# Optimization experiments

Measured on AMD Instinct MI355X. Metric: run time of the kernel, lower is better.

The kernel has to match this reference:

```python
import jax, jax.numpy as jnp
import numpy as np

B, N_GENES, N_SETS, G = 256, 10000, 1000, 128   # batch, input_dim, output_dim, geneset_size
H1, H2 = 64, 32                                  # hidden_dims
EPS = 1e-5                                       # BatchNorm1d eps


def _batchnorm(h, gamma, beta):
    # BatchNorm1d in training mode: biased batch stats over the batch axis
    mean = jnp.mean(h, axis=0, keepdims=True)
    var = jnp.mean(jnp.square(h - mean), axis=0, keepdims=True)
    return (h - mean) * jax.lax.rsqrt(var + EPS) * gamma + beta


def setup_inputs() -> dict:
    key = jax.random.key(0)
    ks = jax.random.split(key, 7)
    # Adjacency with exactly G distinct ones per column -> gather index list [N_SETS, G]
    rng = np.random.default_rng(0)
    gene_idx = np.argsort(rng.random((N_SETS, N_GENES)), axis=1)[:, :G]
    gene_idx = jnp.asarray(np.sort(gene_idx, axis=1), dtype=jnp.int32)

    x = jax.random.normal(ks[0], (B, N_GENES), jnp.float32)
    s1, s2, s3 = 1.0 / np.sqrt(G), 1.0 / np.sqrt(H1), 1.0 / np.sqrt(H2)
    W1 = jax.random.uniform(ks[1], (N_SETS, G, H1), jnp.float32, -s1, s1)
    b1 = jax.random.uniform(ks[2], (N_SETS, H1), jnp.float32, -s1, s1)
    W2 = jax.random.uniform(ks[3], (N_SETS, H1, H2), jnp.float32, -s2, s2)
    b2 = jax.random.uniform(ks[4], (N_SETS, H2), jnp.float32, -s2, s2)
    W3 = jax.random.uniform(ks[5], (N_SETS, H2), jnp.float32, -s3, s3)
    b3 = jax.random.uniform(ks[6], (N_SETS,), jnp.float32, -s3, s3)
    g1 = jnp.ones((N_SETS, H1), jnp.float32)
    be1 = jnp.zeros((N_SETS, H1), jnp.float32)
    g2 = jnp.ones((N_SETS, H2), jnp.float32)
    be2 = jnp.zeros((N_SETS, H2), jnp.float32)
    return {"x": x, "gene_idx": gene_idx, "W1": W1, "b1": b1, "g1": g1, "be1": be1,
            "W2": W2, "b2": b2, "g2": g2, "be2": be2, "W3": W3, "b3": b3}


def reference(x, gene_idx, W1, b1, g1, be1, W2, b2, g2, be2, W3, b3):
    # Per-geneset gather: x[:, adj[:,i]==1] for all i at once -> [B, S, G]
    xg = x[:, gene_idx]
    # Linear -> ReLU -> BatchNorm (per geneset, grouped GEMM)
    h = jax.nn.relu(jnp.einsum('bsg,sgh->bsh', xg, W1) + b1)
    h = _batchnorm(h, g1, be1)
    h = jax.nn.relu(jnp.einsum('bsh,shk->bsk', h, W2) + b2)
    h = _batchnorm(h, g2, be2)
    # Final Linear(H2 -> 1) -> ReLU, concatenated over genesets -> [B, S]
    out = jax.nn.relu(jnp.einsum('bsh,sh->bs', h, W3) + b3)
    return out
```

## Files before the change

### kernel.cpp

```cpp
#include <hip/hip_runtime.h>
#include <stdint.h>

#define BB 256
#define NG 10000
#define NS 1000
#define GG 128
#define H1 64
#define H2 32
#define EPSV 1e-5f


typedef unsigned short ushortT;
typedef __attribute__((ext_vector_type(4))) short short4v;
typedef __attribute__((ext_vector_type(8))) short short8v;
typedef __attribute__((ext_vector_type(4))) float float4v;

__device__ __forceinline__ float bf2f(ushortT u) {
    union { uint32_t i; float f; } v; v.i = ((uint32_t)u) << 16; return v.f;
}
__device__ __forceinline__ ushortT f2bf(float f) {
    union { float f; uint32_t i; } v; v.f = f;
    uint32_t x = v.i;
    return (ushortT)((x + 0x7fffu + ((x >> 16) & 1u)) >> 16);
}
__device__ __forceinline__ uint32_t cvtpk_bf16(float lo, float hi) {
    uint32_t d;
    asm("v_cvt_pk_bf16_f32 %0, %1, %2" : "=v"(d) : "v"(lo), "v"(hi));
    return d;
}
__device__ __forceinline__ uint32_t pack2(ushortT lo, ushortT hi) {
    return (uint32_t)lo | ((uint32_t)hi << 16);
}
__device__ __forceinline__ bool probe_f32(const void* g1) {
    return ((*(const uint32_t*)g1) & 0xFFFFu) == 0u;
}
__device__ __forceinline__ float loadf(const void* p, int i, bool isf) {
    return isf ? ((const float*)p)[i] : bf2f(((const ushortT*)p)[i]);
}
__device__ __forceinline__ ushortT loadbf(const void* p, size_t i, bool isf) {
    return isf ? f2bf(((const float*)p)[i]) : ((const ushortT*)p)[i];
}

__global__ __launch_bounds__(256) void k_transpose(const void* __restrict__ x,
                                                   ushortT* __restrict__ xT,
                                                   const void* __restrict__ g1p) {
    __shared__ ushortT tile[64][66];
    const bool isf = probe_f32(g1p);
    const int q = threadIdx.x & 15;
    const int r = threadIdx.x >> 4;
    const int j0 = blockIdx.x * 64;
    const int b0 = blockIdx.y * 64;
    const bool fullj = (j0 + 64 <= NG);
#pragma unroll
    for (int k = 0; k < 4; ++k) {
        const int bl = k * 16 + r;
        const int jq = q * 4;
        const size_t src = (size_t)(b0 + bl) * NG + j0 + jq;
        uint32_t d0, d1;
        if (isf) {
            if (fullj) {
                float4 v = *(const float4*)((const float*)x + src);
                d0 = cvtpk_bf16(v.x, v.y);
                d1 = cvtpk_bf16(v.z, v.w);
            } else {
                float vx[4];
#pragma unroll
                for (int i2 = 0; i2 < 4; ++i2)
                    vx[i2] = (j0 + jq + i2 < NG) ? ((const float*)x)[src + i2] : 0.f;
                d0 = cvtpk_bf16(vx[0], vx[1]);
                d1 = cvtpk_bf16(vx[2], vx[3]);
            }
        } else {
            if (fullj) {
                uint2 v = *(const uint2*)((const ushortT*)x + src);
                d0 = v.x; d1 = v.y;
            } else {
                ushortT e[4];
#pragma unroll
                for (int i2 = 0; i2 < 4; ++i2)
                    e[i2] = (j0 + jq + i2 < NG) ? ((const ushortT*)x)[src + i2] : (ushortT)0;
                d0 = pack2(e[0], e[1]); d1 = pack2(e[2], e[3]);
            }
        }
        *(uint32_t*)(&tile[bl][jq]) = d0;
        *(uint32_t*)(&tile[bl][jq + 2]) = d1;
    }
    __syncthreads();
#pragma unroll
    for (int k = 0; k < 4; ++k) {
        const int jl = k * 16 + r;
        const int jw = j0 + jl;
        if (jw < NG) {
            const int bq = q * 4;
            uint2 o;
            o.x = pack2(tile[bq + 0][jl], tile[bq + 1][jl]);
            o.y = pack2(tile[bq + 2][jl], tile[bq + 3][jl]);
            *(uint2*)(&xT[(size_t)jw * BB + b0 + bq]) = o;
        }
    }
}

__global__ __launch_bounds__(256, 4) void k_main(
    const ushortT* __restrict__ xT, const int* __restrict__ gidx,
    const void* __restrict__ W1, const void* __restrict__ W2,
    const void* __restrict__ b1, const void* __restrict__ g1, const void* __restrict__ be1,
    const void* __restrict__ b2, const void* __restrict__ g2, const void* __restrict__ be2,
    const void* __restrict__ W3, const void* __restrict__ b3,
    void* __restrict__ out) {
    __shared__ ushortT xg[BB * 68];
    __shared__ ushortT w1s[64 * 36];

    char* xgc = (char*)xg;
    float* redf = (float*)w1s;
    ushortT* w2s = w1s;

    const bool isf = probe_f32(g1);
    const int s = blockIdx.x;
    const int t = threadIdx.x;
    const int w = t >> 6;
    const int lane = t & 63;
    const int l16 = lane & 15;
    const int quad = lane >> 4;
    const size_t base1 = (size_t)s * (GG * H1);
    const size_t base2 = (size_t)s * (H1 * H2);

#define HOLEF(r0, k) (*(float*)(xgc + ((r0) + ((k) >> 1)) * 136 + 128 + ((k) & 1) * 4))

    const int gq = t & 15;
    const int bo2 = t >> 4;
    const int B0 = bo2 * 16;
    int4 gidA = *(const int4*)(gidx + s * GG + 4 * gq);

    const float* W1f = (const float*)W1 + base1;
    const ushortT* W1h = (const ushortT*)W1 + base1;

    uint4 w1A0, w1A1, w1B0, w1B1;
    if (isf) {
        w1A0 = *(const uint4*)(W1f + (size_t)(0 * 512 + 0 * 256 + t) * 4);
        w1A1 = *(const uint4*)(W1f + (size_t)(0 * 512 + 1 * 256 + t) * 4);
    } else {
        w1A0 = *(const uint4*)(W1h + (size_t)0 * 2048 + t * 8);
    }

    float b1v[4];
#pragma unroll
    for (int nt = 0; nt < 4; ++nt) b1v[nt] = loadf(b1, s * H1 + nt * 16 + l16, isf);
    float g1v = 0.f, be1v = 0.f;
    if (t < 64) { g1v = loadf(g1, s * H1 + t, isf); be1v = loadf(be1, s * H1 + t, isf); }

    auto stageF = [&](uint4 vv, int rr) {
        union { uint32_t i; float f; } u0, u1, u2, u3;
        u0.i = vv.x; u1.i = vv.y; u2.i = vv.z; u3.i = vv.w;
        const int g = rr * 16 + (t >> 4);
        const int h0 = (t & 15) * 4;
        const uint32_t p01 = cvtpk_bf16(u0.f, u1.f);
        const uint32_t p23 = cvtpk_bf16(u2.f, u3.f);
        w1s[(h0 + 0) * 36 + g] = (ushortT)p01;
        w1s[(h0 + 1) * 36 + g] = (ushortT)(p01 >> 16);
        w1s[(h0 + 2) * 36 + g] = (ushortT)p23;
        w1s[(h0 + 3) * 36 + g] = (ushortT)(p23 >> 16);
    };
    auto stageU = [&](uint4 vv) {
        const int g = t >> 3;
        const int h0 = (t & 7) * 8;
        w1s[(h0 + 0) * 36 + g] = (ushortT)vv.x;
        w1s[(h0 + 1) * 36 + g] = (ushortT)(vv.x >> 16);
        w1s[(h0 + 2) * 36 + g] = (ushortT)vv.y;
        w1s[(h0 + 3) * 36 + g] = (ushortT)(vv.y >> 16);
        w1s[(h0 + 4) * 36 + g] = (ushortT)vv.z;
        w1s[(h0 + 5) * 36 + g] = (ushortT)(vv.z >> 16);
        w1s[(h0 + 6) * 36 + g] = (ushortT)vv.w;
        w1s[(h0 + 7) * 36 + g] = (ushortT)(vv.w >> 16);
    };

    float4v acc1[4][4];
#pragma unroll
    for (int mt = 0; mt < 4; ++mt)
#pragma unroll
        for (int nt = 0; nt < 4; ++nt) acc1[mt][nt] = (float4v){0.f, 0.f, 0.f, 0.f};

    uint4 gv[8];
    auto gload = [&](const int4 g4) {
        const ushortT* r0 = xT + (size_t)g4.x * BB + B0;
        const ushortT* r1 = xT + (size_t)g4.y * BB + B0;
        const ushortT* r2 = xT + (size_t)g4.z * BB + B0;
        const ushortT* r3 = xT + (size_t)g4.w * BB + B0;
        gv[0] = *(const uint4*)(r0); gv[1] = *(const uint4*)(r0 + 8);
        gv[2] = *(const uint4*)(r1); gv[3] = *(const uint4*)(r1 + 8);
        gv[4] = *(const uint4*)(r2); gv[5] = *(const uint4*)(r2 + 8);
        gv[6] = *(const uint4*)(r3); gv[7] = *(const uint4*)(r3 + 8);
    };
    auto unpack = [&]() {
#pragma unroll
        for (int oc = 0; oc < 2; ++oc) {
            const uint32_t aw[4] = {gv[0 + oc].x, gv[0 + oc].y, gv[0 + oc].z, gv[0 + oc].w};
            const uint32_t bw[4] = {gv[2 + oc].x, gv[2 + oc].y, gv[2 + oc].z, gv[2 + oc].w};
            const uint32_t cw[4] = {gv[4 + oc].x, gv[4 + oc].y, gv[4 + oc].z, gv[4 + oc].w};
            const uint32_t dw[4] = {gv[6 + oc].x, gv[6 + oc].y, gv[6 + oc].z, gv[6 + oc].w};
#pragma unroll
            for (int p = 0; p < 4; ++p) {
#pragma unroll
                for (int hf = 0; hf < 2; ++hf) {
                    const uint32_t sel = hf ? 0x07060302u : 0x05040100u;
                    uint2 o;
                    o.x = __builtin_amdgcn_perm(bw[p], aw[p], sel);
                    o.y = __builtin_amdgcn_perm(dw[p], cw[p], sel);
                    const int b = B0 + oc * 8 + p * 2 + hf;
                    *(uint2*)(&xg[b * 68 + 4 * gq]) = o;
                }
            }
        }
    };
    auto mfmaChunk = [&](int kt) {
        short8v bfrag[4];
#pragma unroll
        for (int nt = 0; nt < 4; ++nt) {
            const int h = nt * 16 + l16;
            const int woff = h * 36 + quad * 8;
            short4v blo = *(const short4v*)(&w1s[woff]);
            short4v bhi = *(const short4v*)(&w1s[woff + 4]);
            bfrag[nt] = __builtin_shufflevector(blo, bhi, 0, 1, 2, 3, 4, 5, 6, 7);
        }
#pragma unroll
        for (int mt = 0; mt < 4; ++mt) {
            const int b = w * 64 + mt * 16 + l16;
            const ushortT* p = &xg[b * 68 + kt * 32 + quad * 8];
            short4v alo = *(const short4v*)(p);
            short4v ahi = *(const short4v*)(p + 4);
            short8v af = __builtin_shufflevector(alo, ahi, 0, 1, 2, 3, 4, 5, 6, 7);
#pragma unroll
            for (int nt = 0; nt < 4; ++nt)
                acc1[mt][nt] = __builtin_amdgcn_mfma_f32_16x16x32_bf16(af, bfrag[nt], acc1[mt][nt], 0, 0, 0);
        }
    };

    gload(gidA);
    unpack();
    int4 gidB = *(const int4*)(gidx + s * GG + 64 + 4 * gq);
    if (isf) { stageF(w1A0, 0); stageF(w1A1, 1); } else { stageU(w1A0); }
    if (isf) {
        w1B0 = *(const uint4*)(W1f + (size_t)(1 * 512 + 0 * 256 + t) * 4);
        w1B1 = *(const uint4*)(W1f + (size_t)(1 * 512 + 1 * 256 + t) * 4);
    } else {
        w1B0 = *(const uint4*)(W1h + (size_t)1 * 2048 + t * 8);
    }
    __syncthreads();
    mfmaChunk(0);
    __syncthreads();
    if (isf) { stageF(w1B0, 0); stageF(w1B1, 1); } else { stageU(w1B0); }
    if (isf) {
        w1A0 = *(const uint4*)(W1f + (size_t)(2 * 512 + 0 * 256 + t) * 4);
        w1A1 = *(const uint4*)(W1f + (size_t)(2 * 512 + 1 * 256 + t) * 4);
    } else {
        w1A0 = *(const uint4*)(W1h + (size_t)2 * 2048 + t * 8);
    }
    __syncthreads();
    mfmaChunk(1);

    gload(gidB);
    __syncthreads();
    unpack();
    if (isf) { stageF(w1A0, 0); stageF(w1A1, 1); } else { stageU(w1A0); }
    if (isf) {
        w1B0 = *(const uint4*)(W1f + (size_t)(3 * 512 + 0 * 256 + t) * 4);
        w1B1 = *(const uint4*)(W1f + (size_t)(3 * 512 + 1 * 256 + t) * 4);
    } else {
        w1B0 = *(const uint4*)(W1h + (size_t)3 * 2048 + t * 8);
    }
    __syncthreads();
    mfmaChunk(0);
    __syncthreads();
    if (isf) { stageF(w1B0, 0); stageF(w1B1, 1); } else { stageU(w1B0); }
    __syncthreads();
    mfmaChunk(1);

    ushortT w2r[8];
    {
        const int k2 = t & 31, h0 = (t >> 5) * 8;
#pragma unroll
        for (int j = 0; j < 8; ++j) w2r[j] = loadbf(W2, base2 + (size_t)(h0 + j) * H2 + k2, isf);
    }
    float b2v[2], w3v[2];
#pragma unroll
    for (int nt = 0; nt < 2; ++nt) {
        b2v[nt] = loadf(b2, s * H2 + nt * 16 + l16, isf);
        w3v[nt] = loadf(W3, s * H2 + nt * 16 + l16, isf);
    }
    const float b3v = loadf(b3, s, isf);
    float g2v = 0.f, be2v = 0.f;
    if (t < 32) { g2v = loadf(g2, s * H2 + t, isf); be2v = loadf(be2, s * H2 + t, isf); }

    float s1v[4], s2v[4];
#pragma unroll
    for (int nt = 0; nt < 4; ++nt) {
        float s1 = 0.f, s2 = 0.f;
        const float bb = b1v[nt];
#pragma unroll
        for (int mt = 0; mt < 4; ++mt)
#pragma unroll
            for (int r = 0; r < 4; ++r) {
                float v = acc1[mt][nt][r] + bb;
                v = v > 0.f ? v : 0.f;
                s1 += v;
                s2 += v * v;
            }
        s1 += __shfl_xor(s1, 16); s1 += __shfl_xor(s1, 32);
        s2 += __shfl_xor(s2, 16); s2 += __shfl_xor(s2, 32);
        s1v[nt] = s1; s2v[nt] = s2;
    }
    __syncthreads();
    if (lane < 16) {
#pragma unroll
        for (int nt = 0; nt < 4; ++nt) {
            const int k = w * 64 + nt * 16 + lane;
            redf[k] = s1v[nt];
            redf[256 + k] = s2v[nt];
        }
    }
    __syncthreads();

    if (t < 64) {
        float ts = redf[t] + redf[64 + t] + redf[128 + t] + redf[192 + t];
        float tq = redf[256 + t] + redf[320 + t] + redf[384 + t] + redf[448 + t];
        float mean = ts * (1.0f / 256.0f);
        float var = tq * (1.0f / 256.0f) - mean * mean;
        var = var > 0.f ? var : 0.f;
        float rs = rsqrtf(var + EPSV);
        float a = g1v * rs;
        HOLEF(64, t) = a;
        HOLEF(96, t) = be1v - mean * a;
    }
    __syncthreads();

    {
        const int k2 = t & 31, h0 = (t >> 5) * 8;
        uint4 pk;
        pk.x = pack2(w2r[0], w2r[1]);
        pk.y = pack2(w2r[2], w2r[3]);
        pk.z = pack2(w2r[4], w2r[5]);
        pk.w = pack2(w2r[6], w2r[7]);
        *(uint4*)(&w2s[k2 * 72 + h0]) = pk;
    }
#pragma unroll
    for (int nt = 0; nt < 4; ++nt) {
        const int h = nt * 16 + l16;
        const float bb = b1v[nt];
        const float a = HOLEF(64, h), cc = HOLEF(96, h);
#pragma unroll
        for (int mt = 0; mt < 4; ++mt) {
            const int b0r = w * 64 + mt * 16 + quad * 4;
#pragma unroll
            for (int rp = 0; rp < 2; ++rp) {
                float v0 = acc1[mt][nt][2 * rp] + bb;     v0 = v0 > 0.f ? v0 : 0.f;
                float v1 = acc1[mt][nt][2 * rp + 1] + bb; v1 = v1 > 0.f ? v1 : 0.f;
                const uint32_t pk = cvtpk_bf16(v0 * a + cc, v1 * a + cc);
                xg[(b0r + 2 * rp) * 68 + h] = (ushortT)pk;
                xg[(b0r + 2 * rp + 1) * 68 + h] = (ushortT)(pk >> 16);
            }
        }
    }
    __syncthreads();

    float4v acc2[4][2];
#pragma unroll
    for (int mt = 0; mt < 4; ++mt)
#pragma unroll
        for (int nt = 0; nt < 2; ++nt) acc2[mt][nt] = (float4v){0.f, 0.f, 0.f, 0.f};

#pragma unroll
    for (int kt = 0; kt < 2; ++kt) {
        const int kl = kt * 32 + quad * 8;
        short8v bfrag2[2];
#pragma unroll
        for (int nt = 0; nt < 2; ++nt) {
            const int k2 = nt * 16 + l16;
            const int woff = k2 * 72 + kl;
            short4v blo = *(const short4v*)(&w2s[woff]);
            short4v bhi = *(const short4v*)(&w2s[woff + 4]);
            bfrag2[nt] = __builtin_shufflevector(blo, bhi, 0, 1, 2, 3, 4, 5, 6, 7);
        }
#pragma unroll
        for (int mt = 0; mt < 4; ++mt) {
            const int b = w * 64 + mt * 16 + l16;
            const ushortT* p = &xg[b * 68 + kl];
            short4v alo = *(const short4v*)(p);
            short4v ahi = *(const short4v*)(p + 4);
            short8v af = __builtin_shufflevector(alo, ahi, 0, 1, 2, 3, 4, 5, 6, 7);
#pragma unroll
            for (int nt = 0; nt < 2; ++nt)
                acc2[mt][nt] = __builtin_amdgcn_mfma_f32_16x16x32_bf16(af, bfrag2[nt], acc2[mt][nt], 0, 0, 0);
        }
    }

#pragma unroll
    for (int nt = 0; nt < 2; ++nt) {
        float s1 = 0.f, s2 = 0.f;
        const float bb = b2v[nt];
#pragma unroll
        for (int mt = 0; mt < 4; ++mt)
#pragma unroll
            for (int r = 0; r < 4; ++r) {
                float v = acc2[mt][nt][r] + bb;
                v = v > 0.f ? v : 0.f;
                s1 += v;
                s2 += v * v;
            }
        s1 += __shfl_xor(s1, 16); s1 += __shfl_xor(s1, 32);
        s2 += __shfl_xor(s2, 16); s2 += __shfl_xor(s2, 32);
        if (lane < 16) {
            const int k = w * 32 + nt * 16 + lane;
            HOLEF(0, k) = s1;
            HOLEF(64, k) = s2;
        }
    }
    __syncthreads();

    if (t < 32) {
        float ts = HOLEF(0, t) + HOLEF(0, 32 + t) + HOLEF(0, 64 + t) + HOLEF(0, 96 + t);
        float tq = HOLEF(64, t) + HOLEF(64, 32 + t) + HOLEF(64, 64 + t) + HOLEF(64, 96 + t);
        float mean = ts * (1.0f / 256.0f);
        float var = tq * (1.0f / 256.0f) - mean * mean;
        var = var > 0.f ? var : 0.f;
        float rs = rsqrtf(var + EPSV);
        float a = g2v * rs;
        HOLEF(128, t) = a;
        HOLEF(144, t) = be2v - mean * a;
    }
    __syncthreads();

    float a2[2], c2[2];
#pragma unroll
    for (int nt = 0; nt < 2; ++nt) {
        const int k2 = nt * 16 + l16;
        a2[nt] = HOLEF(128, k2);
        c2[nt] = HOLEF(144, k2);
    }
#pragma unroll
    for (int mt = 0; mt < 4; ++mt)
#pragma unroll
        for (int r = 0; r < 4; ++r) {
            float tot = 0.f;
#pragma unroll
            for (int nt = 0; nt < 2; ++nt) {
                float v = acc2[mt][nt][r] + b2v[nt];
                v = v > 0.f ? v : 0.f;
                tot += (v * a2[nt] + c2[nt]) * w3v[nt];
            }
            tot += __shfl_xor(tot, 1);
            tot += __shfl_xor(tot, 2);
            tot += __shfl_xor(tot, 4);
            tot += __shfl_xor(tot, 8);
            if (l16 == 0) {
                const int b = w * 64 + mt * 16 + quad * 4 + r;
                float o = tot + b3v;
                o = o > 0.f ? o : 0.f;
                if (isf) ((float*)out)[b * NS + s] = o;
                else     ((ushortT*)out)[b * NS + s] = f2bf(o);
            }
        }
#undef HOLEF
}

extern "C" void kernel_launch(void* const* d_in, const int* in_sizes, int n_in,
                              void* d_out, int out_size, void* d_ws, size_t ws_size,
                              hipStream_t stream) {
    const int* gi = (const int*)d_in[1];
    ushortT* xT = (ushortT*)d_ws;

    dim3 gT((NG + 63) / 64, BB / 64);
    k_transpose<<<gT, 256, 0, stream>>>(d_in[0], xT, d_in[4]);
    k_main<<<NS, 256, 0, stream>>>(xT, gi, d_in[2], d_in[6],
                                   d_in[3], d_in[4], d_in[5],
                                   d_in[7], d_in[8], d_in[9], d_in[10], d_in[11],
                                   d_out);
}
```

Baseline: 134.1 us.

## Prefetch all W1 chunks up front and drop BatchNorm reduction barriers

```diff
diff --git a/kernel.cpp b/kernel.cpp
--- a/kernel.cpp
+++ b/kernel.cpp
@@ -111,7 +111,6 @@
     __shared__ ushortT w1s[64 * 36];
 
     char* xgc = (char*)xg;
-    float* redf = (float*)w1s;
     ushortT* w2s = w1s;
 
     const bool isf = probe_f32(g1);
@@ -124,42 +123,42 @@
     const size_t base1 = (size_t)s * (GG * H1);
     const size_t base2 = (size_t)s * (H1 * H2);
 
-#define HOLEF(r0, k) (*(float*)(xgc + ((r0) + ((k) >> 1)) * 136 + 128 + ((k) & 1) * 4))
+#define HOLE2(r) (*(float2*)(xgc + (r) * 136 + 128))
 
     const int gq = t & 15;
     const int bo2 = t >> 4;
     const int B0 = bo2 * 16;
     int4 gidA = *(const int4*)(gidx + s * GG + 4 * gq);
+    int4 gidB = *(const int4*)(gidx + s * GG + 64 + 4 * gq);
 
     const float* W1f = (const float*)W1 + base1;
     const ushortT* W1h = (const ushortT*)W1 + base1;
 
-    uint4 w1A0, w1A1, w1B0, w1B1;
+    uint4 w1p[4];
     if (isf) {
-        w1A0 = *(const uint4*)(W1f + (size_t)(0 * 512 + 0 * 256 + t) * 4);
-        w1A1 = *(const uint4*)(W1f + (size_t)(0 * 512 + 1 * 256 + t) * 4);
+        float4 ra[4], rb[4];
+#pragma unroll
+        for (int q = 0; q < 4; ++q) {
+            ra[q] = *(const float4*)(W1f + (size_t)q * 2048 + 8 * t);
+            rb[q] = *(const float4*)(W1f + (size_t)q * 2048 + 8 * t + 4);
+        }
+#pragma unroll
+        for (int q = 0; q < 4; ++q) {
+            w1p[q].x = cvtpk_bf16(ra[q].x, ra[q].y);
+            w1p[q].y = cvtpk_bf16(ra[q].z, ra[q].w);
+            w1p[q].z = cvtpk_bf16(rb[q].x, rb[q].y);
+            w1p[q].w = cvtpk_bf16(rb[q].z, rb[q].w);
+        }
     } else {
-        w1A0 = *(const uint4*)(W1h + (size_t)0 * 2048 + t * 8);
+#pragma unroll
+        for (int q = 0; q < 4; ++q)
+            w1p[q] = *(const uint4*)(W1h + (size_t)q * 2048 + 8 * t);
     }
 
     float b1v[4];
 #pragma unroll
     for (int nt = 0; nt < 4; ++nt) b1v[nt] = loadf(b1, s * H1 + nt * 16 + l16, isf);
-    float g1v = 0.f, be1v = 0.f;
-    if (t < 64) { g1v = loadf(g1, s * H1 + t, isf); be1v = loadf(be1, s * H1 + t, isf); }
-
-    auto stageF = [&](uint4 vv, int rr) {
-        union { uint32_t i; float f; } u0, u1, u2, u3;
-        u0.i = vv.x; u1.i = vv.y; u2.i = vv.z; u3.i = vv.w;
-        const int g = rr * 16 + (t >> 4);
-        const int h0 = (t & 15) * 4;
-        const uint32_t p01 = cvtpk_bf16(u0.f, u1.f);
-        const uint32_t p23 = cvtpk_bf16(u2.f, u3.f);
-        w1s[(h0 + 0) * 36 + g] = (ushortT)p01;
-        w1s[(h0 + 1) * 36 + g] = (ushortT)(p01 >> 16);
-        w1s[(h0 + 2) * 36 + g] = (ushortT)p23;
-        w1s[(h0 + 3) * 36 + g] = (ushortT)(p23 >> 16);
-    };
+
     auto stageU = [&](uint4 vv) {
         const int g = t >> 3;
         const int h0 = (t & 7) * 8;
@@ -236,61 +235,55 @@
 
     gload(gidA);
     unpack();
-    int4 gidB = *(const int4*)(gidx + s * GG + 64 + 4 * gq);
-    if (isf) { stageF(w1A0, 0); stageF(w1A1, 1); } else { stageU(w1A0); }
+    stageU(w1p[0]);
+    __syncthreads();
+    mfmaChunk(0);
+    __syncthreads();
+    gload(gidB);
+    stageU(w1p[1]);
+    __syncthreads();
+    mfmaChunk(1);
+    unpack();
+
+    float4 w2fa, w2fb; uint4 w2u;
     if (isf) {
-        w1B0 = *(const uint4*)(W1f + (size_t)(1 * 512 + 0 * 256 + t) * 4);
-        w1B1 = *(const uint4*)(W1f + (size_t)(1 * 512 + 1 * 256 + t) * 4);
+        w2fa = *(const float4*)((const float*)W2 + base2 + 8 * t);
+        w2fb = *(const float4*)((const float*)W2 + base2 + 8 * t + 4);
     } else {
-        w1B0 = *(const uint4*)(W1h + (size_t)1 * 2048 + t * 8);
-    }
+        w2u = *(const uint4*)((const ushortT*)W2 + base2 + 8 * t);
+    }
+
+    __syncthreads();
+    stageU(w1p[2]);
     __syncthreads();
     mfmaChunk(0);
     __syncthreads();
-    if (isf) { stageF(w1B0, 0); stageF(w1B1, 1); } else { stageU(w1B0); }
+    stageU(w1p[3]);
+    __syncthreads();
+    mfmaChunk(1);
+
     if (isf) {
-        w1A0 = *(const uint4*)(W1f + (size_t)(2 * 512 + 0 * 256 + t) * 4);
-        w1A1 = *(const uint4*)(W1f + (size_t)(2 * 512 + 1 * 256 + t) * 4);
-    } else {
-        w1A0 = *(const uint4*)(W1h + (size_t)2 * 2048 + t * 8);
-    }
-    __syncthreads();
-    mfmaChunk(1);
-
-    gload(gidB);
-    __syncthreads();
-    unpack();
-    if (isf) { stageF(w1A0, 0); stageF(w1A1, 1); } else { stageU(w1A0); }
-    if (isf) {
-        w1B0 = *(const uint4*)(W1f + (size_t)(3 * 512 + 0 * 256 + t) * 4);
-        w1B1 = *(const uint4*)(W1f + (size_t)(3 * 512 + 1 * 256 + t) * 4);
-    } else {
-        w1B0 = *(const uint4*)(W1h + (size_t)3 * 2048 + t * 8);
-    }
-    __syncthreads();
-    mfmaChunk(0);
-    __syncthreads();
-    if (isf) { stageF(w1B0, 0); stageF(w1B1, 1); } else { stageU(w1B0); }
-    __syncthreads();
-    mfmaChunk(1);
-
-    ushortT w2r[8];
-    {
-        const int k2 = t & 31, h0 = (t >> 5) * 8;
-#pragma unroll
-        for (int j = 0; j < 8; ++j) w2r[j] = loadbf(W2, base2 + (size_t)(h0 + j) * H2 + k2, isf);
-    }
-    float b2v[2], w3v[2];
+        w2u.x = cvtpk_bf16(w2fa.x, w2fa.y);
+        w2u.y = cvtpk_bf16(w2fa.z, w2fa.w);
+        w2u.z = cvtpk_bf16(w2fb.x, w2fb.y);
+        w2u.w = cvtpk_bf16(w2fb.z, w2fb.w);
+    }
+    float g1a[4], be1a[4];
+#pragma unroll
+    for (int nt = 0; nt < 4; ++nt) {
+        g1a[nt] = loadf(g1, s * H1 + nt * 16 + l16, isf);
+        be1a[nt] = loadf(be1, s * H1 + nt * 16 + l16, isf);
+    }
+    float b2v[2], w3v[2], g2a[2], be2a[2];
 #pragma unroll
     for (int nt = 0; nt < 2; ++nt) {
         b2v[nt] = loadf(b2, s * H2 + nt * 16 + l16, isf);
         w3v[nt] = loadf(W3, s * H2 + nt * 16 + l16, isf);
+        g2a[nt] = loadf(g2, s * H2 + nt * 16 + l16, isf);
+        be2a[nt] = loadf(be2, s * H2 + nt * 16 + l16, isf);
     }
     const float b3v = loadf(b3, s, isf);
-    float g2v = 0.f, be2v = 0.f;
-    if (t < 32) { g2v = loadf(g2, s * H2 + t, isf); be2v = loadf(be2, s * H2 + t, isf); }
-
-    float s1v[4], s2v[4];
+
 #pragma unroll
     for (int nt = 0; nt < 4; ++nt) {
         float s1 = 0.f, s2 = 0.f;
@@ -306,46 +299,37 @@
             }
         s1 += __shfl_xor(s1, 16); s1 += __shfl_xor(s1, 32);
         s2 += __shfl_xor(s2, 16); s2 += __shfl_xor(s2, 32);
-        s1v[nt] = s1; s2v[nt] = s2;
-    }
-    __syncthreads();
-    if (lane < 16) {
-#pragma unroll
-        for (int nt = 0; nt < 4; ++nt) {
-            const int k = w * 64 + nt * 16 + lane;
-            redf[k] = s1v[nt];
-            redf[256 + k] = s2v[nt];
-        }
-    }
-    __syncthreads();
-
-    if (t < 64) {
-        float ts = redf[t] + redf[64 + t] + redf[128 + t] + redf[192 + t];
-        float tq = redf[256 + t] + redf[320 + t] + redf[384 + t] + redf[448 + t];
+        if (lane < 16) HOLE2(w * 64 + nt * 16 + lane) = (float2){s1, s2};
+    }
+    __syncthreads();
+
+    {
+        const int h2 = t >> 2, k0 = (t & 3) * 8;
+        w2s[(k0 + 0) * 72 + h2] = (ushortT)w2u.x;
+        w2s[(k0 + 1) * 72 + h2] = (ushortT)(w2u.x >> 16);
+        w2s[(k0 + 2) * 72 + h2] = (ushortT)w2u.y;
+        w2s[(k0 + 3) * 72 + h2] = (ushortT)(w2u.y >> 16);
+        w2s[(k0 + 4) * 72 + h2] = (ushortT)w2u.z;
+        w2s[(k0 + 5) * 72 + h2] = (ushortT)(w2u.z >> 16);
+        w2s[(k0 + 6) * 72 + h2] = (ushortT)w2u.w;
+        w2s[(k0 + 7) * 72 + h2] = (ushortT)(w2u.w >> 16);
+    }
+#pragma unroll
+    for (int nt = 0; nt < 4; ++nt) {
+        const int h = nt * 16 + l16;
+        float ts = 0.f, tq = 0.f;
+#pragma unroll
+        for (int wv = 0; wv < 4; ++wv) {
+            float2 p = HOLE2(h + 64 * wv);
+            ts += p.x; tq += p.y;
+        }
         float mean = ts * (1.0f / 256.0f);
         float var = tq * (1.0f / 256.0f) - mean * mean;
         var = var > 0.f ? var : 0.f;
         float rs = rsqrtf(var + EPSV);
-        float a = g1v * rs;
-        HOLEF(64, t) = a;
-        HOLEF(96, t) = be1v - mean * a;
-    }
-    __syncthreads();
-
-    {
-        const int k2 = t & 31, h0 = (t >> 5) * 8;
-        uint4 pk;
-        pk.x = pack2(w2r[0], w2r[1]);
-        pk.y = pack2(w2r[2], w2r[3]);
-        pk.z = pack2(w2r[4], w2r[5]);
-        pk.w = pack2(w2r[6], w2r[7]);
-        *(uint4*)(&w2s[k2 * 72 + h0]) = pk;
-    }
-#pragma unroll
-    for (int nt = 0; nt < 4; ++nt) {
-        const int h = nt * 16 + l16;
+        const float a = g1a[nt] * rs;
+        const float cc = be1a[nt] - mean * a;
         const float bb = b1v[nt];
-        const float a = HOLEF(64, h), cc = HOLEF(96, h);
 #pragma unroll
         for (int mt = 0; mt < 4; ++mt) {
             const int b0r = w * 64 + mt * 16 + quad * 4;
@@ -407,33 +391,26 @@
             }
         s1 += __shfl_xor(s1, 16); s1 += __shfl_xor(s1, 32);
         s2 += __shfl_xor(s2, 16); s2 += __shfl_xor(s2, 32);
-        if (lane < 16) {
-            const int k = w * 32 + nt * 16 + lane;
-            HOLEF(0, k) = s1;
-            HOLEF(64, k) = s2;
-        }
-    }
-    __syncthreads();
-
-    if (t < 32) {
-        float ts = HOLEF(0, t) + HOLEF(0, 32 + t) + HOLEF(0, 64 + t) + HOLEF(0, 96 + t);
-        float tq = HOLEF(64, t) + HOLEF(64, 32 + t) + HOLEF(64, 64 + t) + HOLEF(64, 96 + t);
+        if (lane < 16) HOLE2(w * 32 + nt * 16 + lane) = (float2){s1, s2};
+    }
+    __syncthreads();
+
+    float a2[2], c2[2];
+#pragma unroll
+    for (int nt = 0; nt < 2; ++nt) {
+        const int k2 = nt * 16 + l16;
+        float ts = 0.f, tq = 0.f;
+#pragma unroll
+        for (int wv = 0; wv < 4; ++wv) {
+            float2 p = HOLE2(k2 + 32 * wv);
+            ts += p.x; tq += p.y;
+        }
         float mean = ts * (1.0f / 256.0f);
         float var = tq * (1.0f / 256.0f) - mean * mean;
         var = var > 0.f ? var : 0.f;
         float rs = rsqrtf(var + EPSV);
-        float a = g2v * rs;
-        HOLEF(128, t) = a;
-        HOLEF(144, t) = be2v - mean * a;
-    }
-    __syncthreads();
-
-    float a2[2], c2[2];
-#pragma unroll
-    for (int nt = 0; nt < 2; ++nt) {
-        const int k2 = nt * 16 + l16;
-        a2[nt] = HOLEF(128, k2);
-        c2[nt] = HOLEF(144, k2);
+        a2[nt] = g2a[nt] * rs;
+        c2[nt] = be2a[nt] - mean * a2[nt];
     }
 #pragma unroll
     for (int mt = 0; mt < 4; ++mt)
@@ -458,7 +435,7 @@
                 else     ((ushortT*)out)[b * NS + s] = f2bf(o);
             }
         }
-#undef HOLEF
+#undef HOLE2
 }
 
 extern "C" void kernel_launch(void* const* d_in, const int* in_sizes, int n_in,
```

After: 149.6 us. +11.6%, slower.
